# Optimization experiments

Measured on AMD Instinct MI355X. Metric: run time of the kernel, lower is better.

The kernel has to match this reference:

```python
import jax, jax.numpy as jnp
import numpy as np

B = 16
H = 56
W = 56
C = 384
NH = 12
HD = C // NH
WS = 7
SHIFT = 3
N = WS * WS
SCALE = HD ** -0.5
EPS = 1e-3  # keras LayerNormalization default epsilon


def _rel_pos_index():
    coords = np.stack(np.meshgrid(np.arange(WS), np.arange(WS), indexing='ij')).reshape(2, -1)
    rel = (coords[:, :, None] - coords[:, None, :]).transpose(1, 2, 0)
    rel[:, :, 0] += WS - 1
    rel[:, :, 1] += WS - 1
    rel[:, :, 0] *= 2 * WS - 1
    return rel.sum(-1)  # [N, N]

REL_IDX = jnp.asarray(_rel_pos_index())


def _shift_mask():
    # faithful reproduction of the TransformerBlock.__init__ mask construction
    mask = np.zeros((1, H, W, 1), np.float32)
    slices = (slice(0, -WS), slice(-WS, -SHIFT), slice(-SHIFT, None))
    cnt = 0
    for hs in slices:
        for ws in slices:
            mask[:, hs, ws, :] = cnt
            cnt += 1
    mw = mask.reshape(1, H // WS, WS, W // WS, WS, 1).transpose(0, 1, 3, 2, 4, 5).reshape(-1, N)
    m = mw[:, None, :] - mw[:, :, None]  # expand_dims(mw,1) - expand_dims(mw,2)
    return np.where(m != 0, np.float32(-100.0), np.float32(0.0))  # [nw, N, N]

MASK = jnp.asarray(_shift_mask())


def _ln(x, g, b):
    mu = x.mean(-1, keepdims=True)
    var = ((x - mu) ** 2).mean(-1, keepdims=True)
    return (x - mu) / jnp.sqrt(var + EPS) * g + b


def _window_partition(x):  # [B,H,W,C] -> [B*nw, N, C]
    b = x.shape[0]
    x = x.reshape(b, H // WS, WS, W // WS, WS, C).transpose(0, 1, 3, 2, 4, 5)
    return x.reshape(-1, N, C)


def _window_reverse(wins, b):  # [B*nw, WS, WS, C] -> [B,H,W,C]
    x = wins.reshape(b, H // WS, W // WS, WS, WS, C).transpose(0, 1, 3, 2, 4, 5)
    return x.reshape(b, H, W, C)


def setup_inputs() -> dict:
    key = jax.random.key(0)
    ks = jax.random.split(key, 8)
    s = 0.02
    return {
        'x': jax.random.normal(ks[0], (B, H * W, C), jnp.float32),
        'ln1_g': jnp.ones((C,), jnp.float32),
        'ln1_b': jnp.zeros((C,), jnp.float32),
        'ln2_g': jnp.ones((C,), jnp.float32),
        'ln2_b': jnp.zeros((C,), jnp.float32),
        'qkv_w': s * jax.random.normal(ks[1], (C, 3 * C), jnp.float32),
        'qkv_b': jnp.zeros((3 * C,), jnp.float32),
        'proj_w': s * jax.random.normal(ks[2], (C, C), jnp.float32),
        'proj_b': jnp.zeros((C,), jnp.float32),
        'mlp_w1': s * jax.random.normal(ks[3], (C, 4 * C), jnp.float32),
        'mlp_b1': jnp.zeros((4 * C,), jnp.float32),
        'mlp_w2': s * jax.random.normal(ks[4], (4 * C, C), jnp.float32),
        'mlp_b2': jnp.zeros((C,), jnp.float32),
        'rel_pos_table': s * jax.random.normal(ks[5], ((2 * WS - 1) * (2 * WS - 1), NH), jnp.float32),
    }


def reference(x, ln1_g, ln1_b, ln2_g, ln2_b, qkv_w, qkv_b, proj_w, proj_b,
              mlp_w1, mlp_b1, mlp_w2, mlp_b2, rel_pos_table):
    skip = x
    y = _ln(x, ln1_g, ln1_b).reshape(B, H, W, C)
    # cyclic shift (faithful to source: shift=(-s, +s))
    y = jnp.roll(y, shift=(-SHIFT, SHIFT), axis=(1, 2))
    wins = _window_partition(y)                      # [nW, N, C]
    nW = wins.shape[0]

    qkv = wins @ qkv_w + qkv_b                       # [nW, N, 3C]
    qkv = qkv.reshape(nW, N, 3, NH, HD).transpose(2, 0, 3, 1, 4)
    q, k, v = qkv[0] * SCALE, qkv[1], qkv[2]         # [nW, NH, N, HD]

    attn = jnp.einsum('whnd,whmd->whnm', q, k)       # [nW, NH, N, N]
    bias = rel_pos_table[REL_IDX.reshape(-1)].reshape(N, N, NH).transpose(2, 0, 1)
    attn = attn + bias[None]

    nw = MASK.shape[0]
    attn = attn.reshape(nW // nw, nw, NH, N, N) + MASK[None, :, None]
    attn = jax.nn.softmax(attn.reshape(nW, NH, N, N), axis=-1)

    out = jnp.einsum('whnm,whmd->wnhd', attn, v).reshape(nW, N, C)
    out = out @ proj_w + proj_b

    y = _window_reverse(out.reshape(-1, WS, WS, C), B)
    # reverse shift (faithful to source: shift=(+s, +s))
    y = jnp.roll(y, shift=(SHIFT, SHIFT), axis=(1, 2))
    x = y.reshape(B, H * W, C) + skip

    skip = x
    y = _ln(x, ln2_g, ln2_b)
    y = jax.nn.gelu(y @ mlp_w1 + mlp_b1, approximate=False)
    y = y @ mlp_w2 + mlp_b2
    return y + skip
```

## Files before the change

### kernel.cpp

```cpp
#include <hip/hip_runtime.h>
#include <hip/hip_bf16.h>
#include <math.h>

typedef __hip_bfloat16 bf16;
typedef unsigned short ushort_t;
typedef __bf16 bf16x8 __attribute__((ext_vector_type(8)));
typedef float f32x4 __attribute__((ext_vector_type(4)));

#define TOKENS 50176
#define CW2 512
#define CROWS2 (CW2 * 49)
#define SCALE_ 0.17677669529663687f

__device__ __forceinline__ float b2f(bf16 v) { return __bfloat162float(v); }
__device__ __forceinline__ bf16  f2b(float v) { return __float2bfloat16(v); }

__device__ __forceinline__ float gelu_f(float v) {
  float x = v * 0.7071067811865475f;
  float ax = fabsf(x);
  float t = 1.f / (1.f + 0.3275911f * ax);
  float poly = ((((1.061405429f * t - 1.453152027f) * t + 1.421413741f) * t
                 - 0.284496736f) * t + 0.254829592f) * t;
  float erfv = 1.f - poly * __expf(-ax * ax);
  erfv = copysignf(erfv, x);
  return 0.5f * v * (1.f + erfv);
}

__global__ __launch_bounds__(256) void wt_bf16(const float* __restrict__ W,
                                               ushort_t* __restrict__ Wt,
                                               int K, int N) {
  int idx = blockIdx.x * 256 + threadIdx.x;
  if (idx >= K * N) return;
  int n = idx / K, k = idx - n * K;
  bf16 h = f2b(W[(size_t)k * N + n]);
  Wt[idx] = *(ushort_t*)&h;
}

__global__ __launch_bounds__(64) void ln1_kernel(const float* __restrict__ x,
                                                 const float* __restrict__ g,
                                                 const float* __restrict__ bta,
                                                 bf16* __restrict__ wins) {
  int t = blockIdx.x;
  int lane = threadIdx.x;
  int w = t / 49, n = t - w * 49;
  int bi = w >> 6, wi = w & 63;
  int hw = wi >> 3, ww = wi & 7;
  int ti = n / 7, tj = n - ti * 7;
  int hr = hw * 7 + ti, wr = ww * 7 + tj;
  int hs = (hr + 3) % 56;
  int wsc = (wr + 53) % 56;
  const float* row = x + ((size_t)bi * 3136 + hs * 56 + wsc) * 384;
  float v[6];
  float s = 0.f, s2 = 0.f;
#pragma unroll
  for (int j = 0; j < 6; ++j) {
    v[j] = row[lane + 64 * j];
    s += v[j]; s2 += v[j] * v[j];
  }
#pragma unroll
  for (int m = 32; m >= 1; m >>= 1) {
    s  += __shfl_xor(s, m, 64);
    s2 += __shfl_xor(s2, m, 64);
  }
  float mu = s * (1.f / 384.f);
  float var = s2 * (1.f / 384.f) - mu * mu;
  float rstd = rsqrtf(var + 1e-3f);
  bf16* orow = wins + (size_t)t * 384;
#pragma unroll
  for (int j = 0; j < 6; ++j) {
    int c = lane + 64 * j;
    orow[c] = f2b((v[j] - mu) * rstd * g[c] + bta[c]);
  }
}

__global__ __launch_bounds__(64) void ln2_kernel(const float* __restrict__ x1,
                                                 const float* __restrict__ g,
                                                 const float* __restrict__ bta,
                                                 bf16* __restrict__ out) {
  int t = blockIdx.x;
  int lane = threadIdx.x;
  const float* row = x1 + (size_t)t * 384;
  float v[6];
  float s = 0.f, s2 = 0.f;
#pragma unroll
  for (int j = 0; j < 6; ++j) {
    v[j] = row[lane + 64 * j];
    s += v[j]; s2 += v[j] * v[j];
  }
#pragma unroll
  for (int m = 32; m >= 1; m >>= 1) {
    s  += __shfl_xor(s, m, 64);
    s2 += __shfl_xor(s2, m, 64);
  }
  float mu = s * (1.f / 384.f);
  float var = s2 * (1.f / 384.f) - mu * mu;
  float rstd = rsqrtf(var + 1e-3f);
  bf16* orow = out + (size_t)t * 384;
#pragma unroll
  for (int j = 0; j < 6; ++j) {
    int c = lane + 64 * j;
    orow[c] = f2b((v[j] - mu) * rstd * g[c] + bta[c]);
  }
}

template<int MODE>
__global__ __launch_bounds__(256) void mfma_gemm(
    const ushort_t* __restrict__ A, const ushort_t* __restrict__ Bt,
    const float* __restrict__ bias, int N, int K,
    const float* __restrict__ resid, void* __restrict__ out_) {
  __shared__ ushort_t As[3][128 * 32];
  __shared__ ushort_t Bs[3][128 * 32];
  int tid = threadIdx.x;
  int lane = tid & 63, wv = tid >> 6;
  int wm = wv >> 1, wn = wv & 1;
  int lm = lane & 15, kg = lane >> 4;

  int nwg = gridDim.x;
  int q = nwg >> 3, r = nwg & 7;
  int xcd = blockIdx.x & 7, ii = blockIdx.x >> 3;
  int l = ((xcd < r) ? xcd * (q + 1) : r * (q + 1) + (xcd - r) * q) + ii;
  int nxt = N >> 7;
  int col0 = (l % nxt) * 128, row0 = (l / nxt) * 128;

  f32x4 acc[4][4];
#pragma unroll
  for (int i = 0; i < 4; ++i)
#pragma unroll
    for (int j = 0; j < 4; ++j) acc[i][j] = (f32x4){0.f, 0.f, 0.f, 0.f};

  int rsub = lane >> 2;
  int bsrc = (lane & 3) ^ ((rsub >> 1) & 3);
  int pbr = kg ^ ((lm >> 1) & 3);

  auto stage = [&](int t, int buf) {
    int kk0 = t << 5;
#pragma unroll
    for (int ch = 0; ch < 2; ++ch) {
      int c = wv * 2 + ch;
      int rr = c * 16 + rsub;
      const ushort_t* ga = &A[(size_t)(row0 + rr) * K + kk0 + bsrc * 8];
      const ushort_t* gb = &Bt[(size_t)(col0 + rr) * K + kk0 + bsrc * 8];
      __builtin_amdgcn_global_load_lds(
          (const __attribute__((address_space(1))) void*)ga,
          (__attribute__((address_space(3))) void*)&As[buf][c * 512], 16, 0, 0);
      __builtin_amdgcn_global_load_lds(
          (const __attribute__((address_space(1))) void*)gb,
          (__attribute__((address_space(3))) void*)&Bs[buf][c * 512], 16, 0, 0);
    }
  };

  auto compute = [&](int buf) {
    bf16x8 a[4], b[4];
#pragma unroll
    for (int i = 0; i < 4; ++i) {
      int ra = wm * 64 + i * 16 + lm;
      int rb = wn * 64 + i * 16 + lm;
      a[i] = *(const bf16x8*)&As[buf][ra * 32 + pbr * 8];
      b[i] = *(const bf16x8*)&Bs[buf][rb * 32 + pbr * 8];
    }
#pragma unroll
    for (int i = 0; i < 4; ++i)
#pragma unroll
      for (int j = 0; j < 4; ++j)
        acc[i][j] = __builtin_amdgcn_mfma_f32_16x16x32_bf16(a[i], b[j], acc[i][j], 0, 0, 0);
  };

  int NT = K >> 5;
  stage(0, 0);
  stage(1, 1);

  for (int t = 0; t < NT - 1; ++t) {
    asm volatile("s_waitcnt vmcnt(4)" ::: "memory");
    __builtin_amdgcn_sched_barrier(0);
    __builtin_amdgcn_s_barrier();
    if (t + 2 < NT) stage(t + 2, (t + 2) % 3);
    compute(t % 3);
  }
  asm volatile("s_waitcnt vmcnt(0)" ::: "memory");
  __builtin_amdgcn_sched_barrier(0);
  __builtin_amdgcn_s_barrier();
  compute((NT - 1) % 3);

  int m0 = row0 + wm * 64, n0 = col0 + wn * 64;
#pragma unroll
  for (int i = 0; i < 4; ++i) {
#pragma unroll
    for (int reg = 0; reg < 4; ++reg) {
      int m = m0 + i * 16 + kg * 4 + reg;
      size_t obase = 0;
      if (MODE == 1) {
        int w = m / 49, nn = m - w * 49;
        int bi = w >> 6, wi = w & 63;
        int hw = wi >> 3, ww = wi & 7;
        int ti = nn / 7, tj = nn - ti * 7;
        int hf = (hw * 7 + ti + 3) % 56, wf = (ww * 7 + tj + 3) % 56;
        obase = ((size_t)bi * 3136 + hf * 56 + wf) * 384;
      }
#pragma unroll
      for (int j = 0; j < 4; ++j) {
        int cN = n0 + j * 16 + lm;
        float v = acc[i][j][reg] + bias[cN];
        if (MODE == 0) {
          ((bf16*)out_)[(size_t)m * N + cN] = f2b(v);
        } else if (MODE == 1) {
          float* O = (float*)out_;
          O[obase + cN] = v + resid[obase + cN];
        } else if (MODE == 2) {
          ((bf16*)out_)[(size_t)m * N + cN] = f2b(gelu_f(v));
        } else {
          float* O = (float*)out_;
          O[(size_t)m * N + cN] = v + resid[(size_t)m * N + cN];
        }
      }
    }
  }
}

__global__ __launch_bounds__(256) void attn_mfma(const ushort_t* __restrict__ qkv_c,
                                                 const float* __restrict__ table,
                                                 ushort_t* __restrict__ attn_c,
                                                 int w_base) {
  int wl = blockIdx.x >> 2, hg = blockIdx.x & 3;
  int w = w_base + wl;
  int wi = w & 63;
  int hw = wi >> 3, ww = wi & 7;
  __shared__ ushort_t Qs[64 * 40];
  __shared__ ushort_t Ks[64 * 40];
  __shared__ ushort_t Vt[32 * 72];
  __shared__ ushort_t Ps[64 * 72];
  __shared__ float bias_s[169 * 12];
  int tid = threadIdx.x;
  int lane = tid & 63, wv = tid >> 6;
  int lm = lane & 15, kg = lane >> 4;

  for (int i = tid; i < 64 * 40; i += 256) { Qs[i] = 0; Ks[i] = 0; }
  for (int i = tid; i < 32 * 72; i += 256) Vt[i] = 0;
  for (int i = tid; i < 169 * 12; i += 256) bias_s[i] = table[i];
  __syncthreads();

  for (int hh = 0; hh < 3; ++hh) {
    int h = hg * 3 + hh;
    const ushort_t* base = qkv_c + (size_t)wl * 49 * 1152 + h * 32;
    for (int idx = tid; idx < 392; idx += 256) {
      int n = idx >> 3, d0 = (idx & 7) * 4;
      const ushort_t* p = base + (size_t)n * 1152 + d0;
      ushort4 q = *(const ushort4*)(p);
      ushort4 k = *(const ushort4*)(p + 384);
      ushort4 v = *(const ushort4*)(p + 768);
      *(ushort4*)&Qs[n * 40 + d0] = q;
      *(ushort4*)&Ks[n * 40 + d0] = k;
      Vt[(d0 + 0) * 72 + n] = v.x;
      Vt[(d0 + 1) * 72 + n] = v.y;
      Vt[(d0 + 2) * 72 + n] = v.z;
      Vt[(d0 + 3) * 72 + n] = v.w;
    }
    __syncthreads();

    bf16x8 qa = *(const bf16x8*)&Qs[(wv * 16 + lm) * 40 + kg * 8];
    f32x4 sacc[4];
#pragma unroll
    for (int jt = 0; jt < 4; ++jt) {
      bf16x8 kb = *(const bf16x8*)&Ks[(jt * 16 + lm) * 40 + kg * 8];
      sacc[jt] = __builtin_amdgcn_mfma_f32_16x16x32_bf16(
          qa, kb, (f32x4){0.f, 0.f, 0.f, 0.f}, 0, 0, 0);
    }

    int i_base = wv * 16 + kg * 4;
#pragma unroll
    for (int reg = 0; reg < 4; ++reg) {
      int i = i_base + reg;
      int ii = (i < 49) ? i : 0;
      int yi = ii / 7, xi = ii - yi * 7;
      int hri = hw * 7 + yi, wri = ww * 7 + xi;
      int ri = (hri < 49 ? 0 : (hri < 53 ? 1 : 2)) * 3 + (wri < 49 ? 0 : (wri < 53 ? 1 : 2));
      float sv[4];
      float mx = -1e30f;
#pragma unroll
      for (int jt = 0; jt < 4; ++jt) {
        int j = jt * 16 + lm;
        int jj = (j < 49) ? j : 0;
        int yj = jj / 7, xj = jj - yj * 7;
        int hrj = hw * 7 + yj, wrj = ww * 7 + xj;
        int rj = (hrj < 49 ? 0 : (hrj < 53 ? 1 : 2)) * 3 + (wrj < 49 ? 0 : (wrj < 53 ? 1 : 2));
        int ridx = (yi - yj + 6) * 13 + (xi - xj + 6);
        float s = sacc[jt][reg] * SCALE_ + bias_s[ridx * 12 + h] + ((ri == rj) ? 0.f : -100.f);
        sv[jt] = (j < 49) ? s : -1e30f;
        mx = fmaxf(mx, sv[jt]);
      }
#pragma unroll
      for (int msk = 1; msk < 16; msk <<= 1) mx = fmaxf(mx, __shfl_xor(mx, msk, 64));
      float sm = 0.f;
#pragma unroll
      for (int jt = 0; jt < 4; ++jt) {
        float e = ((jt * 16 + lm) < 49) ? __expf(sv[jt] - mx) : 0.f;
        sv[jt] = e; sm += e;
      }
#pragma unroll
      for (int msk = 1; msk < 16; msk <<= 1) sm += __shfl_xor(sm, msk, 64);
      float inv = 1.f / sm;
#pragma unroll
      for (int jt = 0; jt < 4; ++jt) {
        bf16 pb = f2b(sv[jt] * inv);
        Ps[(size_t)i * 72 + jt * 16 + lm] = *(ushort_t*)&pb;
      }
    }
    f32x4 oacc[2] = {(f32x4){0.f, 0.f, 0.f, 0.f}, (f32x4){0.f, 0.f, 0.f, 0.f}};
#pragma unroll
    for (int ks = 0; ks < 2; ++ks) {
      bf16x8 pa = *(const bf16x8*)&Ps[(wv * 16 + lm) * 72 + ks * 32 + kg * 8];
#pragma unroll
      for (int dt = 0; dt < 2; ++dt) {
        bf16x8 vb = *(const bf16x8*)&Vt[(dt * 16 + lm) * 72 + ks * 32 + kg * 8];
        oacc[dt] = __builtin_amdgcn_mfma_f32_16x16x32_bf16(pa, vb, oacc[dt], 0, 0, 0);
      }
    }
#pragma unroll
    for (int reg = 0; reg < 4; ++reg) {
      int r = i_base + reg;
      if (r < 49) {
#pragma unroll
        for (int dt = 0; dt < 2; ++dt) {
          bf16 ob = f2b(oacc[dt][reg]);
          attn_c[((size_t)wl * 49 + r) * 384 + h * 32 + dt * 16 + lm] = *(ushort_t*)&ob;
        }
      }
    }
    __syncthreads();
  }
}

extern "C" void kernel_launch(void* const* d_in, const int* in_sizes, int n_in,
                              void* d_out, int out_size, void* d_ws, size_t ws_size,
                              hipStream_t stream) {
  const float* x      = (const float*)d_in[0];
  const float* ln1_g  = (const float*)d_in[1];
  const float* ln1_b  = (const float*)d_in[2];
  const float* ln2_g  = (const float*)d_in[3];
  const float* ln2_b  = (const float*)d_in[4];
  const float* qkv_w  = (const float*)d_in[5];
  const float* qkv_b  = (const float*)d_in[6];
  const float* proj_w = (const float*)d_in[7];
  const float* proj_b = (const float*)d_in[8];
  const float* mlp_w1 = (const float*)d_in[9];
  const float* mlp_b1 = (const float*)d_in[10];
  const float* mlp_w2 = (const float*)d_in[11];
  const float* mlp_b2 = (const float*)d_in[12];
  const float* rel_tb = (const float*)d_in[13];

  char* ws = (char*)d_ws;
  ushort_t* r0 = (ushort_t*)(ws + 0);
  ushort_t* r1 = (ushort_t*)(ws + 38535168ull);
  ushort_t* wq = (ushort_t*)(ws + 115605504ull);
  ushort_t* wp = wq + 442368;
  ushort_t* w1 = wp + 147456;
  ushort_t* w2 = w1 + 589824;
  float* out = (float*)d_out;

  wt_bf16<<<1728, 256, 0, stream>>>(qkv_w, wq, 384, 1152);
  wt_bf16<<<576, 256, 0, stream>>>(proj_w, wp, 384, 384);
  wt_bf16<<<2304, 256, 0, stream>>>(mlp_w1, w1, 384, 1536);
  wt_bf16<<<2304, 256, 0, stream>>>(mlp_w2, w2, 1536, 384);

  ln1_kernel<<<TOKENS, 64, 0, stream>>>(x, ln1_g, ln1_b, (bf16*)r0);

  for (int c = 0; c < 2; ++c) {
    ushort_t* winc = r0 + (size_t)c * CROWS2 * 384;
    mfma_gemm<0><<<9 * (CROWS2 / 128), 256, 0, stream>>>(
        winc, wq, qkv_b, 1152, 384, nullptr, (void*)r1);
    attn_mfma<<<CW2 * 4, 256, 0, stream>>>(r1, rel_tb, winc, c * CW2);
  }

  mfma_gemm<1><<<3 * (TOKENS / 128), 256, 0, stream>>>(
      r0, wp, proj_b, 384, 384, x, (void*)out);

  ln2_kernel<<<TOKENS, 64, 0, stream>>>(out, ln2_g, ln2_b, (bf16*)r0);

  for (int c = 0; c < 2; ++c) {
    ushort_t* lc = r0 + (size_t)c * CROWS2 * 384;
    float* oc = out + (size_t)c * CROWS2 * 384;
    mfma_gemm<2><<<12 * (CROWS2 / 128), 256, 0, stream>>>(
        lc, w1, mlp_b1, 1536, 384, nullptr, (void*)r1);
    mfma_gemm<3><<<3 * (CROWS2 / 128), 256, 0, stream>>>(
        r1, w2, mlp_b2, 384, 1536, oc, (void*)oc);
  }
}
```

Measured before the change: 686.0 us.

## Enlarge GEMM tiles to 256x128 with 8 waves, BK=64, interleaved prefetch

Rewrites the shared MFMA GEMM to use 512-thread workgroups computing 256x128 output tiles with a K-step of 64, double-buffered LDS, and an XOR swizzle. Global-to-LDS loads for the next tile are interleaved between MFMA groups with barriers and setprio to overlap memory with compute. The aim is more reuse per LDS load and fewer k-iterations, at the cost of larger LDS use (96KB), lower occupancy, and many extra barriers per iteration.

Measured after the change: 685.0 us. About the same (-0.1%).

```diff
diff --git a/kernel.cpp b/kernel.cpp
--- a/kernel.cpp
+++ b/kernel.cpp
@@ -104,12 +104,12 @@
 }
 
 template<int MODE>
-__global__ __launch_bounds__(256) void mfma_gemm(
+__global__ __launch_bounds__(512) void mfma_gemm(
     const ushort_t* __restrict__ A, const ushort_t* __restrict__ Bt,
     const float* __restrict__ bias, int N, int K,
     const float* __restrict__ resid, void* __restrict__ out_) {
-  __shared__ ushort_t As[3][128 * 32];
-  __shared__ ushort_t Bs[3][128 * 32];
+  __shared__ ushort_t As[2][256 * 64];
+  __shared__ ushort_t Bs[2][128 * 64];
   int tid = threadIdx.x;
   int lane = tid & 63, wv = tid >> 6;
   int wm = wv >> 1, wn = wv & 1;
@@ -120,7 +120,7 @@
   int xcd = blockIdx.x & 7, ii = blockIdx.x >> 3;
   int l = ((xcd < r) ? xcd * (q + 1) : r * (q + 1) + (xcd - r) * q) + ii;
   int nxt = N >> 7;
-  int col0 = (l % nxt) * 128, row0 = (l / nxt) * 128;
+  int col0 = (l % nxt) * 128, row0 = (l / nxt) * 256;
 
   f32x4 acc[4][4];
 #pragma unroll
@@ -128,58 +128,81 @@
 #pragma unroll
     for (int j = 0; j < 4; ++j) acc[i][j] = (f32x4){0.f, 0.f, 0.f, 0.f};
 
-  int rsub = lane >> 2;
-  int bsrc = (lane & 3) ^ ((rsub >> 1) & 3);
-  int pbr = kg ^ ((lm >> 1) & 3);
-
-  auto stage = [&](int t, int buf) {
-    int kk0 = t << 5;
-#pragma unroll
-    for (int ch = 0; ch < 2; ++ch) {
-      int c = wv * 2 + ch;
-      int rr = c * 16 + rsub;
-      const ushort_t* ga = &A[(size_t)(row0 + rr) * K + kk0 + bsrc * 8];
-      const ushort_t* gb = &Bt[(size_t)(col0 + rr) * K + kk0 + bsrc * 8];
-      __builtin_amdgcn_global_load_lds(
-          (const __attribute__((address_space(1))) void*)ga,
-          (__attribute__((address_space(3))) void*)&As[buf][c * 512], 16, 0, 0);
-      __builtin_amdgcn_global_load_lds(
-          (const __attribute__((address_space(1))) void*)gb,
-          (__attribute__((address_space(3))) void*)&Bs[buf][c * 512], 16, 0, 0);
-    }
+  int rsub = lane >> 3;
+  int bblk = lane & 7;
+  int bsw = bblk ^ rsub;
+
+  auto stageA = [&](int t, int buf, int ch) {
+    int kk0 = t << 6;
+    int r8 = wv * 32 + ch * 8;
+    const ushort_t* ga = &A[(size_t)(row0 + r8 + rsub) * K + kk0 + bsw * 8];
+    __builtin_amdgcn_global_load_lds(
+        (const __attribute__((address_space(1))) void*)ga,
+        (__attribute__((address_space(3))) void*)&As[buf][r8 * 64], 16, 0, 0);
   };
-
-  auto compute = [&](int buf) {
-    bf16x8 a[4], b[4];
-#pragma unroll
-    for (int i = 0; i < 4; ++i) {
-      int ra = wm * 64 + i * 16 + lm;
-      int rb = wn * 64 + i * 16 + lm;
-      a[i] = *(const bf16x8*)&As[buf][ra * 32 + pbr * 8];
-      b[i] = *(const bf16x8*)&Bs[buf][rb * 32 + pbr * 8];
-    }
-#pragma unroll
-    for (int i = 0; i < 4; ++i)
-#pragma unroll
-      for (int j = 0; j < 4; ++j)
-        acc[i][j] = __builtin_amdgcn_mfma_f32_16x16x32_bf16(a[i], b[j], acc[i][j], 0, 0, 0);
+  auto stageB = [&](int t, int buf, int ch) {
+    int kk0 = t << 6;
+    int r8 = wv * 16 + ch * 8;
+    const ushort_t* gb = &Bt[(size_t)(col0 + r8 + rsub) * K + kk0 + bsw * 8];
+    __builtin_amdgcn_global_load_lds(
+        (const __attribute__((address_space(1))) void*)gb,
+        (__attribute__((address_space(3))) void*)&Bs[buf][r8 * 64], 16, 0, 0);
   };
 
-  int NT = K >> 5;
-  stage(0, 0);
-  stage(1, 1);
-
-  for (int t = 0; t < NT - 1; ++t) {
-    asm volatile("s_waitcnt vmcnt(4)" ::: "memory");
-    __builtin_amdgcn_sched_barrier(0);
-    __builtin_amdgcn_s_barrier();
-    if (t + 2 < NT) stage(t + 2, (t + 2) % 3);
-    compute(t % 3);
-  }
+  bf16x8 a[4], b[2];
+  auto rdA = [&](int buf, int kk) {
+#pragma unroll
+    for (int i2 = 0; i2 < 4; ++i2) {
+      int ra = wm * 64 + i2 * 16 + lm;
+      a[i2] = *(const bf16x8*)&As[buf][ra * 64 + (((kk * 4 + kg) ^ (ra & 7)) << 3)];
+    }
+  };
+  auto rdB = [&](int buf, int kk, int j, int slot) {
+    int rb = wn * 64 + j * 16 + lm;
+    b[slot] = *(const bf16x8*)&Bs[buf][rb * 64 + (((kk * 4 + kg) ^ (rb & 7)) << 3)];
+  };
+  auto mmac = [&](int jp) {
+    __builtin_amdgcn_s_setprio(1);
+#pragma unroll
+    for (int i2 = 0; i2 < 4; ++i2) {
+      acc[i2][jp * 2 + 0] = __builtin_amdgcn_mfma_f32_16x16x32_bf16(a[i2], b[0], acc[i2][jp * 2 + 0], 0, 0, 0);
+      acc[i2][jp * 2 + 1] = __builtin_amdgcn_mfma_f32_16x16x32_bf16(a[i2], b[1], acc[i2][jp * 2 + 1], 0, 0, 0);
+    }
+    __builtin_amdgcn_s_setprio(0);
+  };
+
+  int NT = K >> 6;
+#pragma unroll
+  for (int ch = 0; ch < 4; ++ch) stageA(0, 0, ch);
+  stageB(0, 0, 0); stageB(0, 0, 1);
   asm volatile("s_waitcnt vmcnt(0)" ::: "memory");
   __builtin_amdgcn_sched_barrier(0);
   __builtin_amdgcn_s_barrier();
-  compute((NT - 1) % 3);
+
+  for (int t = 0; t < NT; ++t) {
+    int buf = t & 1;
+    bool pf = (t + 1 < NT);
+    rdA(buf, 0); rdB(buf, 0, 0, 0); rdB(buf, 0, 1, 1);
+    if (pf) { stageA(t + 1, buf ^ 1, 0); stageA(t + 1, buf ^ 1, 1); stageA(t + 1, buf ^ 1, 2); }
+    __builtin_amdgcn_s_barrier();
+    mmac(0);
+    __builtin_amdgcn_s_barrier();
+    rdB(buf, 0, 2, 0); rdB(buf, 0, 3, 1);
+    if (pf) { stageA(t + 1, buf ^ 1, 3); stageB(t + 1, buf ^ 1, 0); stageB(t + 1, buf ^ 1, 1); }
+    __builtin_amdgcn_s_barrier();
+    mmac(1);
+    __builtin_amdgcn_s_barrier();
+    rdA(buf, 1); rdB(buf, 1, 0, 0); rdB(buf, 1, 1, 1);
+    __builtin_amdgcn_s_barrier();
+    mmac(0);
+    __builtin_amdgcn_s_barrier();
+    rdB(buf, 1, 2, 0); rdB(buf, 1, 3, 1);
+    __builtin_amdgcn_s_barrier();
+    mmac(1);
+    asm volatile("s_waitcnt vmcnt(0)" ::: "memory");
+    __builtin_amdgcn_sched_barrier(0);
+    __builtin_amdgcn_s_barrier();
+  }
 
   int m0 = row0 + wm * 64, n0 = col0 + wn * 64;
 #pragma unroll
@@ -365,12 +388,12 @@
 
   for (int c = 0; c < 2; ++c) {
     ushort_t* winc = r0 + (size_t)c * CROWS2 * 384;
-    mfma_gemm<0><<<9 * (CROWS2 / 128), 256, 0, stream>>>(
+    mfma_gemm<0><<<(CROWS2 / 256) * 9, 512, 0, stream>>>(
         winc, wq, qkv_b, 1152, 384, nullptr, (void*)r1);
     attn_mfma<<<CW2 * 4, 256, 0, stream>>>(r1, rel_tb, winc, c * CW2);
   }
 
-  mfma_gemm<1><<<3 * (TOKENS / 128), 256, 0, stream>>>(
+  mfma_gemm<1><<<(TOKENS / 256) * 3, 512, 0, stream>>>(
       r0, wp, proj_b, 384, 384, x, (void*)out);
 
   ln2_kernel<<<TOKENS, 64, 0, stream>>>(out, ln2_g, ln2_b, (bf16*)r0);
@@ -378,9 +401,9 @@
   for (int c = 0; c < 2; ++c) {
     ushort_t* lc = r0 + (size_t)c * CROWS2 * 384;
     float* oc = out + (size_t)c * CROWS2 * 384;
-    mfma_gemm<2><<<12 * (CROWS2 / 128), 256, 0, stream>>>(
+    mfma_gemm<2><<<(CROWS2 / 256) * 12, 512, 0, stream>>>(
         lc, w1, mlp_b1, 1536, 384, nullptr, (void*)r1);
-    mfma_gemm<3><<<3 * (CROWS2 / 128), 256, 0, stream>>>(
+    mfma_gemm<3><<<(CROWS2 / 256) * 3, 512, 0, stream>>>(
         r1, w2, mlp_b2, 384, 1536, oc, (void*)oc);
   }
 }
```
